# Kernel tuning notes

Hardware: AMD Instinct MI355X
Metric: run time of the kernel (lower is better)

Reference implementation:

```python
import jax, jax.numpy as jnp
import numpy as np

ED = 1024   # encoder_dim
GH = 1024   # gnn_hidden
NL = 3      # gnn_layers
NH = 8      # gnn_heads
HD = GH // NH
N = 2048    # graph nodes
B = 1024    # query/doc batch
TEMP = 0.05
LAPW = 0.1

def _layernorm(x, g, b):
    mu = jnp.mean(x, axis=-1, keepdims=True)
    var = jnp.mean((x - mu) ** 2, axis=-1, keepdims=True)
    return (x - mu) * jax.lax.rsqrt(var + 1e-5) * g + b

def _mlp_proj(x, W1, b1, g, beta, W2, b2):
    h = _layernorm(x @ W1 + b1, g, beta)
    h = jax.nn.gelu(h, approximate=False)
    return h @ W2 + b2

def _l2norm(x):
    n = jnp.linalg.norm(x, axis=-1, keepdims=True)
    return x / jnp.maximum(n, 1e-12)

def _gnn(x, adj, gatW, a1, a2, ln_g, ln_b, poW, pob):
    mask = adj > 0
    for l in range(NL):
        Wh = jnp.einsum('nf,hfo->hno', x, gatW[l])            # [H,N,HD]
        # a([Wh_i, Wh_j]) == Wh_i@a1 + Wh_j@a2 (linear, no bias): avoids NxNx2F concat
        s1 = jnp.einsum('hno,ho->hn', Wh, a1[l])
        s2 = jnp.einsum('hno,ho->hn', Wh, a2[l])
        e = jax.nn.leaky_relu(s1[:, :, None] + s2[:, None, :], 0.2)  # [H,N,N]
        att = jax.nn.softmax(jnp.where(mask[None], e, -9e15), axis=-1)
        h = jnp.einsum('hnm,hmo->hno', att, Wh)               # [H,N,HD]
        h = jnp.transpose(h, (1, 0, 2)).reshape(x.shape[0], GH)  # concat heads
        h = jax.nn.elu(_layernorm(h, ln_g[l], ln_b[l]))
        x = x + h  # in_features == hidden so residual applies every layer
    return x @ poW + pob

def _forward(query_embeds, pos_doc_embeds, node_embeds, adj, laplacian, params):
    (qW1, qb1, qg, qbt, qW2, qb2,
     dW1, db1, dg, dbt, dW2, db2,
     gatW, a1, a2, ln_g, ln_b, poW, pob) = params
    graph_embeds = _gnn(node_embeds, adj, gatW, a1, a2, ln_g, ln_b, poW, pob)
    q = _l2norm(_mlp_proj(query_embeds, qW1, qb1, qg, qbt, qW2, qb2))
    p = _l2norm(_mlp_proj(pos_doc_embeds, dW1, db1, dg, dbt, dW2, db2))
    pos_sim = jnp.sum(q * p, axis=-1) / TEMP                  # [B]
    neg_sim = (q @ p.T) / TEMP                                # [B,B]
    logits = jnp.concatenate([pos_sim[:, None], neg_sim], axis=1)
    info_nce = jnp.mean(jax.nn.logsumexp(logits, axis=-1) - logits[:, 0])
    lap = jnp.sum(graph_embeds * (laplacian @ graph_embeds)) / graph_embeds.shape[0]
    return info_nce + LAPW * lap, info_nce, lap

def setup_inputs() -> dict:
    key = jax.random.key(0)
    ks = jax.random.split(key, 24)
    r = lambda k, s: jax.random.normal(k, s, jnp.float32) * 0.02
    adj = (jax.random.uniform(ks[3], (N, N)) < 0.02).astype(jnp.float32)
    adj = jnp.maximum(adj, jnp.eye(N, dtype=jnp.float32))
    return {
        'query_embeds': jax.random.normal(ks[0], (B, ED), jnp.float32),
        'pos_doc_embeds': jax.random.normal(ks[1], (B, ED), jnp.float32),
        'node_embeds': jax.random.normal(ks[2], (N, ED), jnp.float32),
        'adj': adj,
        'laplacian': r(ks[4], (N, N)),
        'qW1': r(ks[5], (ED, ED)), 'qb1': jnp.zeros((ED,), jnp.float32),
        'qg': jnp.ones((ED,), jnp.float32), 'qbt': jnp.zeros((ED,), jnp.float32),
        'qW2': r(ks[6], (ED, ED)), 'qb2': jnp.zeros((ED,), jnp.float32),
        'dW1': r(ks[7], (ED, ED)), 'db1': jnp.zeros((ED,), jnp.float32),
        'dg': jnp.ones((ED,), jnp.float32), 'dbt': jnp.zeros((ED,), jnp.float32),
        'dW2': r(ks[8], (ED, ED)), 'db2': jnp.zeros((ED,), jnp.float32),
        'gatW': r(ks[9], (NL, NH, ED, HD)),
        'a1': r(ks[10], (NL, NH, HD)),
        'a2': r(ks[11], (NL, NH, HD)),
        'ln_g': jnp.ones((NL, GH), jnp.float32),
        'ln_b': jnp.zeros((NL, GH), jnp.float32),
        'poW': r(ks[12], (GH, ED)),
        'pob': jnp.zeros((ED,), jnp.float32),
    }

def reference(query_embeds, pos_doc_embeds, node_embeds, adj, laplacian,
              qW1, qb1, qg, qbt, qW2, qb2,
              dW1, db1, dg, dbt, dW2, db2,
              gatW, a1, a2, ln_g, ln_b, poW, pob):
    params = (qW1, qb1, qg, qbt, qW2, qb2,
              dW1, db1, dg, dbt, dW2, db2,
              gatW, a1, a2, ln_g, ln_b, poW, pob)
    return _forward(query_embeds, pos_doc_embeds, node_embeds, adj, laplacian, params)
```

## Files before the change

kernel.cpp:

```cpp
#include <hip/hip_runtime.h>
#include <math.h>

#define ED    1024
#define GH    1024
#define NLAY  3
#define NHEAD 8
#define HD    128
#define NNODE 2048
#define BQ    1024
#define CAP   192
#define CAPP  208

typedef unsigned short u16;
typedef __attribute__((ext_vector_type(8))) short short8;
typedef __attribute__((ext_vector_type(4))) float f32x4;

static const size_t OFF_X    = 0;
static const size_t OFF_XB   = 2097152;
static const size_t OFF_WHB  = 3145728;
static const size_t OFF_WTG  = 4194304;
static const size_t OFF_WTPO = 5767168;
static const size_t OFF_WTQ1 = 6291456;
static const size_t OFF_WTD1 = 6815744;
static const size_t OFF_WTQ2 = 7340032;
static const size_t OFF_WTD2 = 7864320;
static const size_t OFF_GB   = 8388608;
static const size_t OFF_QPB  = 11534336;
static const size_t OFF_HF   = 12582912;
static const size_t OFF_HB   = 14680064;
static const size_t OFF_FF   = 15728640;
static const size_t OFF_FB   = 17825792;
static const size_t OFF_NEG  = 18874368;
static const size_t OFF_SV1  = 19922944;
static const size_t OFF_SV2  = 19939328;
static const size_t OFF_ACC  = 19955712;
static const size_t OFF_CNT  = 19955714;
static const size_t OFF_NCNT = 19955720;
static const size_t OFF_NBR  = 19957768;

__device__ __forceinline__ u16 f2bf(float f) {
  unsigned int u = __float_as_uint(f);
  return (u16)((u + 0x7fffu + ((u >> 16) & 1u)) >> 16);
}
__device__ __forceinline__ float bf2f(u16 u) {
  return __uint_as_float(((unsigned int)u) << 16);
}

__device__ __forceinline__ float waveSum(float v) {
#pragma unroll
  for (int off = 32; off; off >>= 1) v += __shfl_xor(v, off, 64);
  return v;
}
__device__ __forceinline__ float waveMax(float v) {
#pragma unroll
  for (int off = 32; off; off >>= 1) v = fmaxf(v, __shfl_xor(v, off, 64));
  return v;
}
__device__ __forceinline__ float blockSum(float v) {
  __shared__ float buf[4];
  int lane = threadIdx.x & 63, wid = threadIdx.x >> 6, nw = (blockDim.x + 63) >> 6;
  v = waveSum(v);
  __syncthreads();
  if (lane == 0) buf[wid] = v;
  __syncthreads();
  float r = buf[0];
  for (int i = 1; i < nw; ++i) r += buf[i];
  return r;
}
__device__ __forceinline__ float blockMax(float v) {
  __shared__ float buf[4];
  int lane = threadIdx.x & 63, wid = threadIdx.x >> 6, nw = (blockDim.x + 63) >> 6;
  v = waveMax(v);
  __syncthreads();
  if (lane == 0) buf[wid] = v;
  __syncthreads();
  float r = buf[0];
  for (int i = 1; i < nw; ++i) r = fmaxf(r, buf[i]);
  return r;
}

#define SWZ(row, seg) (((seg) ^ (((row) >> 1) & 3)) << 3)

__global__ __launch_bounds__(256) void gemm128(
    const u16* __restrict__ A, const u16* __restrict__ B0,
    const u16* __restrict__ B1, float* __restrict__ C, u16* __restrict__ Cb,
    const float* __restrict__ bias0, const float* __restrict__ bias1,
    int M, int N, int K, int split, float scale) {
  __shared__ u16 As[2][128][32];
  __shared__ u16 Bs[2][128][32];
  const int tid = threadIdx.x, wave = tid >> 6, lane = tid & 63;
  const int bm = blockIdx.y * 128, bn = blockIdx.x * 128;
  const u16* Bt = (bm < split) ? B0 : B1;
  const float* bias = (bm < split) ? bias0 : bias1;

  const int sr = tid >> 2, ss = tid & 3;
  const int so = SWZ(sr, ss);
  const u16* ga0 = A  + (size_t)(bm + sr) * K + ss * 8;
  const u16* ga1 = A  + (size_t)(bm + sr + 64) * K + ss * 8;
  const u16* gb0 = Bt + (size_t)(bn + sr) * K + ss * 8;
  const u16* gb1 = Bt + (size_t)(bn + sr + 64) * K + ss * 8;

  const int r16 = lane & 15, kg = lane >> 4;
  const int wm = (wave >> 1) * 64, wn = (wave & 1) * 64;

  f32x4 acc[4][4] = {};
  const int nk = K >> 5;

  float4 pa0 = *(const float4*)ga0;
  float4 pa1 = *(const float4*)ga1;
  float4 pb0 = *(const float4*)gb0;
  float4 pb1 = *(const float4*)gb1;

  for (int kt = 0; kt < nk; ++kt) {
    const int p = kt & 1;
    *(float4*)&As[p][sr][so]      = pa0;
    *(float4*)&As[p][sr + 64][so] = pa1;
    *(float4*)&Bs[p][sr][so]      = pb0;
    *(float4*)&Bs[p][sr + 64][so] = pb1;
    __syncthreads();
    if (kt + 1 < nk) {
      ga0 += 32; ga1 += 32; gb0 += 32; gb1 += 32;
      pa0 = *(const float4*)ga0;
      pa1 = *(const float4*)ga1;
      pb0 = *(const float4*)gb0;
      pb1 = *(const float4*)gb1;
    }
    short8 av[4], bv[4];
#pragma unroll
    for (int i = 0; i < 4; ++i) {
      int row = wm + i * 16 + r16;
      av[i] = *(const short8*)&As[p][row][SWZ(row, kg)];
    }
#pragma unroll
    for (int j = 0; j < 4; ++j) {
      int col = wn + j * 16 + r16;
      bv[j] = *(const short8*)&Bs[p][col][SWZ(col, kg)];
    }
#pragma unroll
    for (int i = 0; i < 4; ++i)
#pragma unroll
      for (int j = 0; j < 4; ++j)
        acc[i][j] = __builtin_amdgcn_mfma_f32_16x16x32_bf16(av[i], bv[j], acc[i][j], 0, 0, 0);
  }

  if (C) {
#pragma unroll
    for (int j = 0; j < 4; ++j) {
      int col = bn + wn + j * 16 + r16;
      float bvv = bias ? bias[col] : 0.f;
#pragma unroll
      for (int i = 0; i < 4; ++i) {
        int row0 = bm + wm + i * 16 + kg * 4;
        float* cp = C + (size_t)row0 * N + col;
#pragma unroll
        for (int r = 0; r < 4; ++r)
          cp[(size_t)r * N] = acc[i][j][r] * scale + bvv;
      }
    }
  }
  if (Cb) {
#pragma unroll
    for (int j = 0; j < 4; ++j) {
      int col = bn + wn + j * 16 + r16;
      float bvv = bias ? bias[col] : 0.f;
#pragma unroll
      for (int i = 0; i < 4; ++i) {
        int row0 = bm + wm + i * 16 + kg * 4;
        u16* cp = Cb + (size_t)row0 * N + col;
#pragma unroll
        for (int r = 0; r < 4; ++r)
          cp[(size_t)r * N] = f2bf(acc[i][j][r] * scale + bvv);
      }
    }
  }
}

__global__ __launch_bounds__(256) void gemm_dual(
    const u16* __restrict__ A0, const u16* __restrict__ B00,
    const u16* __restrict__ B01, float* __restrict__ C0, u16* __restrict__ D0,
    const float* __restrict__ e0, const float* __restrict__ f0, int M0, int sp0, float sc0,
    const float* __restrict__ A1v, const float* __restrict__ A2v,
    float* __restrict__ S1o, float* __restrict__ S2o,
    const u16* __restrict__ A1, const u16* __restrict__ B10,
    const u16* __restrict__ B11, float* __restrict__ C1, u16* __restrict__ D1,
    const float* __restrict__ e1, const float* __restrict__ f1, int M1, int sp1, float sc1) {
  const int z = blockIdx.z;
  const u16* A   = z ? A1 : A0;
  const u16* Bt0 = z ? B10 : B00;
  const u16* Bt1 = z ? B11 : B01;
  float* C = z ? C1 : C0;
  u16*   D = z ? D1 : D0;
  const float* bias0 = z ? e1 : e0;
  const float* bias1 = z ? f1 : f0;
  const int M = z ? M1 : M0, split = z ? sp1 : sp0;
  const float scale = z ? sc1 : sc0;
  const int bm = blockIdx.y * 128, bn = blockIdx.x * 128;
  if (bm >= M) return;
  const int N = 1024, K = 1024;
  const u16* Bt = (bm < split) ? Bt0 : Bt1;
  const float* bias = (bm < split) ? bias0 : bias1;

  __shared__ u16 As[2][128][32];
  __shared__ u16 Bs[2][128][32];
  const int tid = threadIdx.x, wave = tid >> 6, lane = tid & 63;
  const int sr = tid >> 2, ss = tid & 3;
  const int so = SWZ(sr, ss);
  const u16* ga0 = A  + (size_t)(bm + sr) * K + ss * 8;
  const u16* ga1 = A  + (size_t)(bm + sr + 64) * K + ss * 8;
  const u16* gb0 = Bt + (size_t)(bn + sr) * K + ss * 8;
  const u16* gb1 = Bt + (size_t)(bn + sr + 64) * K + ss * 8;
  const int r16 = lane & 15, kg = lane >> 4;
  const int wm = (wave >> 1) * 64, wn = (wave & 1) * 64;

  f32x4 acc[4][4] = {};
  const int nk = 32;

  float4 pa0 = *(const float4*)ga0;
  float4 pa1 = *(const float4*)ga1;
  float4 pb0 = *(const float4*)gb0;
  float4 pb1 = *(const float4*)gb1;

  for (int kt = 0; kt < nk; ++kt) {
    const int p = kt & 1;
    *(float4*)&As[p][sr][so]      = pa0;
    *(float4*)&As[p][sr + 64][so] = pa1;
    *(float4*)&Bs[p][sr][so]      = pb0;
    *(float4*)&Bs[p][sr + 64][so] = pb1;
    __syncthreads();
    if (kt + 1 < nk) {
      ga0 += 32; ga1 += 32; gb0 += 32; gb1 += 32;
      pa0 = *(const float4*)ga0;
      pa1 = *(const float4*)ga1;
      pb0 = *(const float4*)gb0;
      pb1 = *(const float4*)gb1;
    }
    short8 av[4], bv[4];
#pragma unroll
    for (int i = 0; i < 4; ++i) {
      int row = wm + i * 16 + r16;
      av[i] = *(const short8*)&As[p][row][SWZ(row, kg)];
    }
#pragma unroll
    for (int j = 0; j < 4; ++j) {
      int col = wn + j * 16 + r16;
      bv[j] = *(const short8*)&Bs[p][col][SWZ(col, kg)];
    }
#pragma unroll
    for (int i = 0; i < 4; ++i)
#pragma unroll
      for (int j = 0; j < 4; ++j)
        acc[i][j] = __builtin_amdgcn_mfma_f32_16x16x32_bf16(av[i], bv[j], acc[i][j], 0, 0, 0);
  }

  if (C) {
#pragma unroll
    for (int j = 0; j < 4; ++j) {
      int col = bn + wn + j * 16 + r16;
      float bvv = bias ? bias[col] : 0.f;
#pragma unroll
      for (int i = 0; i < 4; ++i) {
        int row0 = bm + wm + i * 16 + kg * 4;
        float* cp = C + (size_t)row0 * N + col;
#pragma unroll
        for (int r = 0; r < 4; ++r)
          cp[(size_t)r * N] = acc[i][j][r] * scale + bvv;
      }
    }
  }
  if (D) {
#pragma unroll
    for (int j = 0; j < 4; ++j) {
      int col = bn + wn + j * 16 + r16;
      float bvv = bias ? bias[col] : 0.f;
#pragma unroll
      for (int i = 0; i < 4; ++i) {
        int row0 = bm + wm + i * 16 + kg * 4;
        u16* cp = D + (size_t)row0 * N + col;
#pragma unroll
        for (int r = 0; r < 4; ++r)
          cp[(size_t)r * N] = f2bf(acc[i][j][r] * scale + bvv);
      }
    }
  }

  if (z == 0 && S1o) {
    float c1[4], c2[4];
#pragma unroll
    for (int j = 0; j < 4; ++j) {
      int col = bn + wn + j * 16 + r16;
      c1[j] = A1v[col]; c2[j] = A2v[col];
    }
    float r1[4][4], r2[4][4];
#pragma unroll
    for (int i = 0; i < 4; ++i)
#pragma unroll
      for (int r = 0; r < 4; ++r) {
        float v1 = 0.f, v2 = 0.f;
#pragma unroll
        for (int j = 0; j < 4; ++j) {
          v1 += acc[i][j][r] * c1[j];
          v2 += acc[i][j][r] * c2[j];
        }
#pragma unroll
        for (int off = 8; off; off >>= 1) {
          v1 += __shfl_xor(v1, off, 64);
          v2 += __shfl_xor(v2, off, 64);
        }
        r1[i][r] = v1; r2[i][r] = v2;
      }
    __syncthreads();
    float* sb1 = (float*)&As[0][0][0];
    float* sb2 = sb1 + 256;
    if (r16 == 0) {
      int half = wn >> 6;
#pragma unroll
      for (int i = 0; i < 4; ++i)
#pragma unroll
        for (int r = 0; r < 4; ++r) {
          int row = wm + i * 16 + kg * 4 + r;
          sb1[half * 128 + row] = r1[i][r];
          sb2[half * 128 + row] = r2[i][r];
        }
    }
    __syncthreads();
    if (tid < 128) {
      int h = blockIdx.x;
      S1o[(h << 11) + bm + tid] = sb1[tid] + sb1[128 + tid];
      S2o[(h << 11) + bm + tid] = sb2[tid] + sb2[128 + tid];
    }
  }
}

__global__ __launch_bounds__(256) void ggt_dot(
    const u16* __restrict__ Gb, const float* __restrict__ L,
    float* __restrict__ acc, int* __restrict__ cnt_done, float* __restrict__ out) {
  __shared__ u16 As[2][128][32];
  __shared__ u16 Bs[2][128][32];
  const int tid = threadIdx.x, wave = tid >> 6, lane = tid & 63;
  const int ti = blockIdx.x & 15, tj = blockIdx.x >> 4;
  const int bm = ti * 128, bn = tj * 128;

  const int sr = tid >> 2, ss = tid & 3;
  const int so = SWZ(sr, ss);
  const u16* ga0 = Gb + (size_t)(bm + sr) * ED + ss * 8;
  const u16* ga1 = Gb + (size_t)(bm + sr + 64) * ED + ss * 8;
  const u16* gb0 = Gb + (size_t)(bn + sr) * ED + ss * 8;
  const u16* gb1 = Gb + (size_t)(bn + sr + 64) * ED + ss * 8;

  const int r16 = lane & 15, kg = lane >> 4;
  const int wm = (wave >> 1) * 64, wn = (wave & 1) * 64;

  f32x4 acc_r[4][4] = {};
  const int nk = 32;

  float4 pa0 = *(const float4*)ga0;
  float4 pa1 = *(const float4*)ga1;
  float4 pb0 = *(const float4*)gb0;
  float4 pb1 = *(const float4*)gb1;

  for (int kt = 0; kt < nk; ++kt) {
    const int p = kt & 1;
    *(float4*)&As[p][sr][so]      = pa0;
    *(float4*)&As[p][sr + 64][so] = pa1;
    *(float4*)&Bs[p][sr][so]      = pb0;
    *(float4*)&Bs[p][sr + 64][so] = pb1;
    __syncthreads();
    if (kt + 1 < nk) {
      ga0 += 32; ga1 += 32; gb0 += 32; gb1 += 32;
      pa0 = *(const float4*)ga0;
      pa1 = *(const float4*)ga1;
      pb0 = *(const float4*)gb0;
      pb1 = *(const float4*)gb1;
    }
    short8 av[4], bv[4];
#pragma unroll
    for (int i = 0; i < 4; ++i) {
      int row = wm + i * 16 + r16;
      av[i] = *(const short8*)&As[p][row][SWZ(row, kg)];
    }
#pragma unroll
    for (int j = 0; j < 4; ++j) {
      int col = wn + j * 16 + r16;
      bv[j] = *(const short8*)&Bs[p][col][SWZ(col, kg)];
    }
#pragma unroll
    for (int i = 0; i < 4; ++i)
#pragma unroll
      for (int j = 0; j < 4; ++j)
        acc_r[i][j] = __builtin_amdgcn_mfma_f32_16x16x32_bf16(av[i], bv[j], acc_r[i][j], 0, 0, 0);
  }

  float sum = 0.f;
#pragma unroll
  for (int i = 0; i < 4; ++i) {
#pragma unroll
    for (int r = 0; r < 4; ++r) {
      int ig = bm + wm + i * 16 + kg * 4 + r;
      const float* lp = L + (size_t)ig * NNODE + bn + wn + r16;
#pragma unroll
      for (int j = 0; j < 4; ++j)
        sum += acc_r[i][j][r] * lp[j * 16];
    }
  }
  sum = blockSum(sum);
  if (tid == 0) {
    atomicAdd(acc, sum);
    __threadfence();
    int prev = atomicAdd(cnt_done, 1);
    if (prev == (int)gridDim.x - 1) {
      float lap  = atomicAdd(acc, 0.f) / 2048.f;
      float info = atomicAdd(acc + 1, 0.f) / 1024.f;
      out[0] = info + 0.1f * lap;
      out[1] = info;
      out[2] = lap;
    }
  }
}

__global__ __launch_bounds__(256) void att_elem(
    const u16* __restrict__ WHb, const float* __restrict__ S1,
    const float* __restrict__ S2, const int* __restrict__ nbr,
    const int* __restrict__ ncnt, float* __restrict__ X, u16* __restrict__ Xb,
    const float* __restrict__ g, const float* __restrict__ b,
    int mode, const float* __restrict__ EIN, u16* __restrict__ EOUT,
    const float* __restrict__ g0, const float* __restrict__ b0,
    const float* __restrict__ g1, const float* __restrict__ b1,
    float* __restrict__ acc) {
  const int t = threadIdx.x;
  if (blockIdx.x < NNODE) {
    __shared__ int snb[CAPP];
    __shared__ float pw[NHEAD][CAPP];
    const int n = blockIdx.x;
    const int h = t >> 5, l = t & 31;
    const int cnt = ncnt[n];
    const int cntP = (cnt + 15) & ~15;
    for (int j = t; j < cnt; j += 256) snb[j] = nbr[n * CAP + j];
    __syncthreads();
    for (int j = cnt + t; j < cntP; j += 256) snb[j] = snb[0];

    const float s1v = S1[(h << 11) + n];
    float ev[6];
    float lmax = -1e30f;
    int ne = 0;
    for (int j = l; j < cnt; j += 32) {
      float e = s1v + S2[(h << 11) + snb[j]];
      e = e > 0.f ? e : 0.2f * e;
      ev[ne++] = e;
      lmax = fmaxf(lmax, e);
    }
#pragma unroll
    for (int off = 16; off; off >>= 1) lmax = fmaxf(lmax, __shfl_xor(lmax, off, 64));
    float lsum = 0.f;
    ne = 0;
    for (int j = l; j < cnt; j += 32) {
      float p = __expf(ev[ne++] - lmax);
      pw[h][j] = p;
      lsum += p;
    }
    for (int j = cnt + l; j < cntP; j += 32) pw[h][j] = 0.f;
#pragma unroll
    for (int off = 16; off; off >>= 1) lsum += __shfl_xor(lsum, off, 64);
    const float inv = 1.f / lsum;
    __syncthreads();

    float o0 = 0.f, o1 = 0.f, o2 = 0.f, o3 = 0.f;
    const u16* wp = WHb + (t << 2);
    for (int j0 = 0; j0 < cntP; j0 += 16) {
      ushort4 buf[16];
#pragma unroll
      for (int u = 0; u < 16; ++u)
        buf[u] = *(const ushort4*)(wp + ((size_t)snb[j0 + u] << 10));
#pragma unroll
      for (int u = 0; u < 16; ++u) {
        float w = pw[h][j0 + u];
        o0 += w * bf2f(buf[u].x);
        o1 += w * bf2f(buf[u].y);
        o2 += w * bf2f(buf[u].z);
        o3 += w * bf2f(buf[u].w);
      }
    }
    o0 *= inv; o1 *= inv; o2 *= inv; o3 *= inv;

    float s  = o0 + o1 + o2 + o3;
    float sq = o0 * o0 + o1 * o1 + o2 * o2 + o3 * o3;
    float mean = blockSum(s) * (1.f / 1024.f);
    float var  = blockSum(sq) * (1.f / 1024.f) - mean * mean;
    float rstd = rsqrtf(fmaxf(var, 0.f) + 1e-5f);
    float4 xv = *(float4*)&X[((size_t)n << 10) + (t << 2)];
    float ov[4] = {o0, o1, o2, o3};
    float xa[4] = {xv.x, xv.y, xv.z, xv.w};
#pragma unroll
    for (int i = 0; i < 4; ++i) {
      int c = (t << 2) + i;
      float y = (ov[i] - mean) * rstd * g[c] + b[c];
      y = y > 0.f ? y : expm1f(y);
      xa[i] += y;
    }
    *(float4*)&X[((size_t)n << 10) + (t << 2)] = make_float4(xa[0], xa[1], xa[2], xa[3]);
    ushort4 o;
    o.x = f2bf(xa[0]); o.y = f2bf(xa[1]); o.z = f2bf(xa[2]); o.w = f2bf(xa[3]);
    *(ushort4*)&Xb[((size_t)n << 10) + (t << 2)] = o;
  } else {
    const int row = blockIdx.x - NNODE;
    if (mode == 0) {
      const float* gg = (row < 1024) ? g0 : g1;
      const float* bb = (row < 1024) ? b0 : b1;
      float4 v = *(const float4*)&EIN[((size_t)row << 10) + (t << 2)];
      float s = v.x + v.y + v.z + v.w;
      float sq = v.x * v.x + v.y * v.y + v.z * v.z + v.w * v.w;
      float mean = blockSum(s) * (1.f / 1024.f);
      float var = blockSum(sq) * (1.f / 1024.f) - mean * mean;
      float rstd = rsqrtf(fmaxf(var, 0.f) + 1e-5f);
      float vals[4] = {v.x, v.y, v.z, v.w};
      ushort4 o;
      u16* oa = (u16*)&o;
#pragma unroll
      for (int i = 0; i < 4; ++i) {
        int c = (t << 2) + i;
        float y = (vals[i] - mean) * rstd * gg[c] + bb[c];
        y = 0.5f * y * (1.f + erff(y * 0.70710678118654752f));
        oa[i] = f2bf(y);
      }
      *(ushort4*)&EOUT[((size_t)row << 10) + (t << 2)] = o;
    } else if (mode == 1) {
      float4 v = *(const float4*)&EIN[((size_t)row << 10) + (t << 2)];
      float sq = v.x * v.x + v.y * v.y + v.z * v.z + v.w * v.w;
      float s = blockSum(sq);
      float inv = 1.f / fmaxf(sqrtf(s), 1e-12f);
      ushort4 o;
      o.x = f2bf(v.x * inv); o.y = f2bf(v.y * inv);
      o.z = f2bf(v.z * inv); o.w = f2bf(v.w * inv);
      *(ushort4*)&EOUT[((size_t)row << 10) + (t << 2)] = o;
    } else {
      const float* rw = EIN + ((size_t)row << 10);
      float4 v = *(const float4*)&rw[t << 2];
      float lm = fmaxf(fmaxf(v.x, v.y), fmaxf(v.z, v.w));
      float m = blockMax(lm);
      float ls = __expf(v.x - m) + __expf(v.y - m) + __expf(v.z - m) + __expf(v.w - m);
      float ssum = blockSum(ls);
      if (t == 0) {
        float pos = rw[row];
        float loss = m + logf(ssum + __expf(pos - m)) - pos;
        atomicAdd(acc + 1, loss);
      }
    }
  }
}

__global__ __launch_bounds__(256) void prep_mega(
    const float* __restrict__ adj, int* __restrict__ nbr, int* __restrict__ ncnt,
    float* __restrict__ acc, int* __restrict__ cnt_done,
    const float* __restrict__ nodes, float* __restrict__ Xf, u16* __restrict__ Xb,
    const float* __restrict__ q, const float* __restrict__ d, u16* __restrict__ QPb) {
  const int bx = blockIdx.x, tid = threadIdx.x;
  if (bx < NNODE) {
    __shared__ int cnt;
    if (bx == 0 && tid < 2) acc[tid] = 0.f;
    if (bx == 0 && tid == 2) *cnt_done = 0;
    if (tid == 0) cnt = 0;
    __syncthreads();
    for (int c = tid; c < NNODE; c += 256) {
      if (adj[((size_t)bx << 11) + c] > 0.f) {
        int p = atomicAdd(&cnt, 1);
        if (p < CAP) nbr[bx * CAP + p] = c;
      }
    }
    __syncthreads();
    if (tid == 0) ncnt[bx] = cnt < CAP ? cnt : CAP;
  } else if (bx < 2 * NNODE) {
    int i = (bx - NNODE) * 256 + tid;
    float4 v = ((const float4*)nodes)[i];
    ((float4*)Xf)[i] = v;
    ushort4 o;
    o.x = f2bf(v.x); o.y = f2bf(v.y); o.z = f2bf(v.z); o.w = f2bf(v.w);
    ((ushort4*)Xb)[i] = o;
  } else {
    int i = (bx - 2 * NNODE) * 256 + tid;
    const int half = BQ * ED / 4;
    const float* src = (i < half) ? q : d;
    int j = (i < half) ? i : i - half;
    float4 v = ((const float4*)src)[j];
    ushort4 o;
    o.x = f2bf(v.x); o.y = f2bf(v.y); o.z = f2bf(v.z); o.w = f2bf(v.w);
    ((ushort4*)QPb)[i] = o;
  }
}

__device__ __forceinline__ void cvt_tr_body(const float* ip, u16* op, int R, int C) {
  __shared__ float T[64][65];
  int r0 = blockIdx.y * 64, c0 = blockIdx.x * 64;
  int t = threadIdx.x;
#pragma unroll
  for (int p = 0; p < 4; ++p) {
    int row = p * 16 + (t >> 4), col = (t & 15) * 4;
    float4 v = *(const float4*)&ip[(size_t)(r0 + row) * C + c0 + col];
    T[row][col] = v.x; T[row][col + 1] = v.y;
    T[row][col + 2] = v.z; T[row][col + 3] = v.w;
  }
  __syncthreads();
#pragma unroll
  for (int p = 0; p < 4; ++p) {
    int c = p * 16 + (t >> 4), r = (t & 15) * 4;
    ushort4 o;
    o.x = f2bf(T[r][c]); o.y = f2bf(T[r + 1][c]);
    o.z = f2bf(T[r + 2][c]); o.w = f2bf(T[r + 3][c]);
    *(ushort4*)&op[(size_t)(c0 + c) * R + r0 + r] = o;
  }
}

__global__ __launch_bounds__(256) void cvt_transpose(
    const float* __restrict__ in, u16* __restrict__ out,
    int R, int C, long inb, long outb) {
  cvt_tr_body(in + (size_t)blockIdx.z * inb, out + (size_t)blockIdx.z * outb, R, C);
}

__global__ __launch_bounds__(256) void cvt_transpose5(
    const float* __restrict__ i0, u16* __restrict__ o0,
    const float* __restrict__ i1, u16* __restrict__ o1,
    const float* __restrict__ i2, u16* __restrict__ o2,
    const float* __restrict__ i3, u16* __restrict__ o3,
    const float* __restrict__ i4, u16* __restrict__ o4) {
  const float* in; u16* out;
  switch (blockIdx.z) {
    case 0: in = i0; out = o0; break;
    case 1: in = i1; out = o1; break;
    case 2: in = i2; out = o2; break;
    case 3: in = i3; out = o3; break;
    default: in = i4; out = o4; break;
  }
  cvt_tr_body(in, out, 1024, 1024);
}

extern "C" void kernel_launch(void* const* d_in, const int* in_sizes, int n_in,
                              void* d_out, int out_size, void* d_ws, size_t ws_size,
                              hipStream_t stream) {
  const float* query = (const float*)d_in[0];
  const float* docs  = (const float*)d_in[1];
  const float* nodes = (const float*)d_in[2];
  const float* adj   = (const float*)d_in[3];
  const float* lapl  = (const float*)d_in[4];
  const float* qW1 = (const float*)d_in[5],  *qb1 = (const float*)d_in[6];
  const float* qg  = (const float*)d_in[7],  *qbt = (const float*)d_in[8];
  const float* qW2 = (const float*)d_in[9],  *qb2 = (const float*)d_in[10];
  const float* dW1 = (const float*)d_in[11], *db1 = (const float*)d_in[12];
  const float* dg  = (const float*)d_in[13], *dbt = (const float*)d_in[14];
  const float* dW2 = (const float*)d_in[15], *db2 = (const float*)d_in[16];
  const float* gatW = (const float*)d_in[17];
  const float* a1   = (const float*)d_in[18];
  const float* a2   = (const float*)d_in[19];
  const float* ln_g = (const float*)d_in[20];
  const float* ln_b = (const float*)d_in[21];
  const float* poW  = (const float*)d_in[22];
  const float* pob  = (const float*)d_in[23];
  float* out = (float*)d_out;

  float* ws = (float*)d_ws;
  float* X    = ws + OFF_X;
  u16*   Xb   = (u16*)(ws + OFF_XB);
  u16*   WHb  = (u16*)(ws + OFF_WHB);
  u16*   WtG  = (u16*)(ws + OFF_WTG);
  u16*   WtPO = (u16*)(ws + OFF_WTPO);
  u16*   WtQ1 = (u16*)(ws + OFF_WTQ1);
  u16*   WtD1 = (u16*)(ws + OFF_WTD1);
  u16*   WtQ2 = (u16*)(ws + OFF_WTQ2);
  u16*   WtD2 = (u16*)(ws + OFF_WTD2);
  u16*   Gb   = (u16*)(ws + OFF_GB);
  u16*   QPb  = (u16*)(ws + OFF_QPB);
  float* Hf   = ws + OFF_HF;
  u16*   Hb   = (u16*)(ws + OFF_HB);
  float* Ff   = ws + OFF_FF;
  u16*   Fb   = (u16*)(ws + OFF_FB);
  float* NEG  = ws + OFF_NEG;
  float* S1v  = ws + OFF_SV1;
  float* S2v  = ws + OFF_SV2;
  float* ACC  = ws + OFF_ACC;
  int*   CNTD = (int*)(ws + OFF_CNT);
  int*   NCNT = (int*)(ws + OFF_NCNT);
  int*   NBR  = (int*)(ws + OFF_NBR);

  const size_t WSL = (size_t)GH * ED;

  prep_mega<<<3 * NNODE, 256, 0, stream>>>(
      adj, NBR, NCNT, ACC, CNTD, nodes, X, Xb, query, docs, QPb);
  cvt_transpose<<<dim3(2, 16, 24), 256, 0, stream>>>(
      gatW, WtG, ED, HD, (long)ED * HD, (long)HD * ED);
  cvt_transpose5<<<dim3(16, 16, 5), 256, 0, stream>>>(
      poW, WtPO, qW1, WtQ1, dW1, WtD1, qW2, WtQ2, dW2, WtD2);

  gemm_dual<<<dim3(8, 16, 2), 256, 0, stream>>>(
      Xb, WtG, WtG, nullptr, WHb, nullptr, nullptr, NNODE, NNODE, 1.f,
      a1, a2, S1v, S2v,
      QPb, WtQ1, WtD1, Hf, nullptr, qb1, db1, 2 * BQ, BQ, 1.f);
  att_elem<<<NNODE + 2 * BQ, 256, 0, stream>>>(
      WHb, S1v, S2v, NBR, NCNT, X, Xb, ln_g, ln_b,
      0, Hf, Hb, qg, qbt, dg, dbt, ACC);

  gemm_dual<<<dim3(8, 16, 2), 256, 0, stream>>>(
      Xb, WtG + WSL, WtG + WSL, nullptr, WHb, nullptr, nullptr, NNODE, NNODE, 1.f,
      a1 + NHEAD * HD, a2 + NHEAD * HD, S1v, S2v,
      Hb, WtQ2, WtD2, Ff, nullptr, qb2, db2, 2 * BQ, BQ, 1.f);
  att_elem<<<NNODE + 2 * BQ, 256, 0, stream>>>(
      WHb, S1v, S2v, NBR, NCNT, X, Xb, ln_g + GH, ln_b + GH,
      1, Ff, Fb, nullptr, nullptr, nullptr, nullptr, ACC);

  gemm_dual<<<dim3(8, 16, 2), 256, 0, stream>>>(
      Xb, WtG + 2 * WSL, WtG + 2 * WSL, nullptr, WHb, nullptr, nullptr, NNODE, NNODE, 1.f,
      a1 + 2 * NHEAD * HD, a2 + 2 * NHEAD * HD, S1v, S2v,
      Fb, Fb + (size_t)BQ * ED, Fb + (size_t)BQ * ED, NEG, nullptr,
      nullptr, nullptr, BQ, BQ, 20.f);
  att_elem<<<NNODE + BQ, 256, 0, stream>>>(
      WHb, S1v, S2v, NBR, NCNT, X, Xb, ln_g + 2 * GH, ln_b + 2 * GH,
      2, NEG, nullptr, nullptr, nullptr, nullptr, nullptr, ACC);

  gemm128<<<dim3(ED / 128, NNODE / 128), 256, 0, stream>>>(
      Xb, WtPO, WtPO, nullptr, Gb, pob, pob, NNODE, ED, GH, NNODE, 1.f);
  ggt_dot<<<256, 256, 0, stream>>>(Gb, lapl, ACC, CNTD, out);
}
```

Baseline: 372.6 us.

## Prefetch two K-tiles ahead in GEMM loops and split-K the Laplacian dot kernel

Every GEMM main loop now keeps two register stages of global loads in flight instead of one. The barrier moves after the next prefetch is issued, so memory latency overlaps more of the MFMA work. ggt_dot is split along K into two halves with a 2D grid, which doubles its block count for better occupancy. The partial sums still combine through the existing atomic accumulation, and the completion counter now checks against the full grid size. The extra prefetch stage adds register pressure.

```diff
diff --git a/kernel.cpp b/kernel.cpp
--- a/kernel.cpp
+++ b/kernel.cpp
@@ -106,25 +106,25 @@
   f32x4 acc[4][4] = {};
   const int nk = K >> 5;
 
-  float4 pa0 = *(const float4*)ga0;
-  float4 pa1 = *(const float4*)ga1;
-  float4 pb0 = *(const float4*)gb0;
-  float4 pb1 = *(const float4*)gb1;
+  float4 xa0 = *(const float4*)ga0, xa1 = *(const float4*)ga1;
+  float4 xb0 = *(const float4*)gb0, xb1 = *(const float4*)gb1;
+  ga0 += 32; ga1 += 32; gb0 += 32; gb1 += 32;
+  float4 ya0 = *(const float4*)ga0, ya1 = *(const float4*)ga1;
+  float4 yb0 = *(const float4*)gb0, yb1 = *(const float4*)gb1;
 
   for (int kt = 0; kt < nk; ++kt) {
     const int p = kt & 1;
-    *(float4*)&As[p][sr][so]      = pa0;
-    *(float4*)&As[p][sr + 64][so] = pa1;
-    *(float4*)&Bs[p][sr][so]      = pb0;
-    *(float4*)&Bs[p][sr + 64][so] = pb1;
-    __syncthreads();
-    if (kt + 1 < nk) {
+    *(float4*)&As[p][sr][so]      = xa0;
+    *(float4*)&As[p][sr + 64][so] = xa1;
+    *(float4*)&Bs[p][sr][so]      = xb0;
+    *(float4*)&Bs[p][sr + 64][so] = xb1;
+    xa0 = ya0; xa1 = ya1; xb0 = yb0; xb1 = yb1;
+    if (kt + 2 < nk) {
       ga0 += 32; ga1 += 32; gb0 += 32; gb1 += 32;
-      pa0 = *(const float4*)ga0;
-      pa1 = *(const float4*)ga1;
-      pb0 = *(const float4*)gb0;
-      pb1 = *(const float4*)gb1;
-    }
+      ya0 = *(const float4*)ga0; ya1 = *(const float4*)ga1;
+      yb0 = *(const float4*)gb0; yb1 = *(const float4*)gb1;
+    }
+    __syncthreads();
     short8 av[4], bv[4];
 #pragma unroll
     for (int i = 0; i < 4; ++i) {
@@ -215,25 +215,25 @@
   f32x4 acc[4][4] = {};
   const int nk = 32;
 
-  float4 pa0 = *(const float4*)ga0;
-  float4 pa1 = *(const float4*)ga1;
-  float4 pb0 = *(const float4*)gb0;
-  float4 pb1 = *(const float4*)gb1;
+  float4 xa0 = *(const float4*)ga0, xa1 = *(const float4*)ga1;
+  float4 xb0 = *(const float4*)gb0, xb1 = *(const float4*)gb1;
+  ga0 += 32; ga1 += 32; gb0 += 32; gb1 += 32;
+  float4 ya0 = *(const float4*)ga0, ya1 = *(const float4*)ga1;
+  float4 yb0 = *(const float4*)gb0, yb1 = *(const float4*)gb1;
 
   for (int kt = 0; kt < nk; ++kt) {
     const int p = kt & 1;
-    *(float4*)&As[p][sr][so]      = pa0;
-    *(float4*)&As[p][sr + 64][so] = pa1;
-    *(float4*)&Bs[p][sr][so]      = pb0;
-    *(float4*)&Bs[p][sr + 64][so] = pb1;
-    __syncthreads();
-    if (kt + 1 < nk) {
+    *(float4*)&As[p][sr][so]      = xa0;
+    *(float4*)&As[p][sr + 64][so] = xa1;
+    *(float4*)&Bs[p][sr][so]      = xb0;
+    *(float4*)&Bs[p][sr + 64][so] = xb1;
+    xa0 = ya0; xa1 = ya1; xb0 = yb0; xb1 = yb1;
+    if (kt + 2 < nk) {
       ga0 += 32; ga1 += 32; gb0 += 32; gb1 += 32;
-      pa0 = *(const float4*)ga0;
-      pa1 = *(const float4*)ga1;
-      pb0 = *(const float4*)gb0;
-      pb1 = *(const float4*)gb1;
-    }
+      ya0 = *(const float4*)ga0; ya1 = *(const float4*)ga1;
+      yb0 = *(const float4*)gb0; yb1 = *(const float4*)gb1;
+    }
+    __syncthreads();
     short8 av[4], bv[4];
 #pragma unroll
     for (int i = 0; i < 4; ++i) {
@@ -339,39 +339,40 @@
   const int tid = threadIdx.x, wave = tid >> 6, lane = tid & 63;
   const int ti = blockIdx.x & 15, tj = blockIdx.x >> 4;
   const int bm = ti * 128, bn = tj * 128;
+  const int k0 = blockIdx.y * 512;
 
   const int sr = tid >> 2, ss = tid & 3;
   const int so = SWZ(sr, ss);
-  const u16* ga0 = Gb + (size_t)(bm + sr) * ED + ss * 8;
-  const u16* ga1 = Gb + (size_t)(bm + sr + 64) * ED + ss * 8;
-  const u16* gb0 = Gb + (size_t)(bn + sr) * ED + ss * 8;
-  const u16* gb1 = Gb + (size_t)(bn + sr + 64) * ED + ss * 8;
+  const u16* ga0 = Gb + (size_t)(bm + sr) * ED + k0 + ss * 8;
+  const u16* ga1 = Gb + (size_t)(bm + sr + 64) * ED + k0 + ss * 8;
+  const u16* gb0 = Gb + (size_t)(bn + sr) * ED + k0 + ss * 8;
+  const u16* gb1 = Gb + (size_t)(bn + sr + 64) * ED + k0 + ss * 8;
 
   const int r16 = lane & 15, kg = lane >> 4;
   const int wm = (wave >> 1) * 64, wn = (wave & 1) * 64;
 
   f32x4 acc_r[4][4] = {};
-  const int nk = 32;
-
-  float4 pa0 = *(const float4*)ga0;
-  float4 pa1 = *(const float4*)ga1;
-  float4 pb0 = *(const float4*)gb0;
-  float4 pb1 = *(const float4*)gb1;
+  const int nk = 16;
+
+  float4 xa0 = *(const float4*)ga0, xa1 = *(const float4*)ga1;
+  float4 xb0 = *(const float4*)gb0, xb1 = *(const float4*)gb1;
+  ga0 += 32; ga1 += 32; gb0 += 32; gb1 += 32;
+  float4 ya0 = *(const float4*)ga0, ya1 = *(const float4*)ga1;
+  float4 yb0 = *(const float4*)gb0, yb1 = *(const float4*)gb1;
 
   for (int kt = 0; kt < nk; ++kt) {
     const int p = kt & 1;
-    *(float4*)&As[p][sr][so]      = pa0;
-    *(float4*)&As[p][sr + 64][so] = pa1;
-    *(float4*)&Bs[p][sr][so]      = pb0;
-    *(float4*)&Bs[p][sr + 64][so] = pb1;
-    __syncthreads();
-    if (kt + 1 < nk) {
+    *(float4*)&As[p][sr][so]      = xa0;
+    *(float4*)&As[p][sr + 64][so] = xa1;
+    *(float4*)&Bs[p][sr][so]      = xb0;
+    *(float4*)&Bs[p][sr + 64][so] = xb1;
+    xa0 = ya0; xa1 = ya1; xb0 = yb0; xb1 = yb1;
+    if (kt + 2 < nk) {
       ga0 += 32; ga1 += 32; gb0 += 32; gb1 += 32;
-      pa0 = *(const float4*)ga0;
-      pa1 = *(const float4*)ga1;
-      pb0 = *(const float4*)gb0;
-      pb1 = *(const float4*)gb1;
-    }
+      ya0 = *(const float4*)ga0; ya1 = *(const float4*)ga1;
+      yb0 = *(const float4*)gb0; yb1 = *(const float4*)gb1;
+    }
+    __syncthreads();
     short8 av[4], bv[4];
 #pragma unroll
     for (int i = 0; i < 4; ++i) {
@@ -407,7 +408,7 @@
     atomicAdd(acc, sum);
     __threadfence();
     int prev = atomicAdd(cnt_done, 1);
-    if (prev == (int)gridDim.x - 1) {
+    if (prev == (int)(gridDim.x * gridDim.y) - 1) {
       float lap  = atomicAdd(acc, 0.f) / 2048.f;
       float info = atomicAdd(acc + 1, 0.f) / 1024.f;
       out[0] = info + 0.1f * lap;
@@ -714,5 +715,5 @@
 
   gemm128<<<dim3(ED / 128, NNODE / 128), 256, 0, stream>>>(
       Xb, WtPO, WtPO, nullptr, Gb, pob, pob, NNODE, ED, GH, NNODE, 1.f);
-  ggt_dot<<<256, 256, 0, stream>>>(Gb, lapl, ACC, CNTD, out);
-}
+  ggt_dot<<<dim3(256, 2), 256, 0, stream>>>(Gb, lapl, ACC, CNTD, out);
+}
```

Result: faster. 353.7 us (-5.1%).
